# Kernel optimization log

Measured on AMD Instinct MI355X. Metric: run time of the kernel, lower is better.

The kernel has to match this reference:

```python
import jax, jax.numpy as jnp
import numpy as np

NUM_TOKENS = 4096
HIDDEN = 2048
INTER = 1408
NUM_EXPERTS = 8
TOP_K = 2


def setup_inputs() -> dict:
    key = jax.random.key(0)
    k1, k2, k3, k4, k5 = jax.random.split(key, 5)
    hidden_states = jax.random.normal(k1, (NUM_TOKENS, HIDDEN), dtype=jnp.float32)
    # w1: (E, 2*I, H) gate+up fused; w2: (E, H, I)
    w1 = jax.random.normal(k2, (NUM_EXPERTS, 2 * INTER, HIDDEN), dtype=jnp.float32) * (1.0 / np.sqrt(HIDDEN))
    w2 = jax.random.normal(k3, (NUM_EXPERTS, HIDDEN, INTER), dtype=jnp.float32) * (1.0 / np.sqrt(INTER))
    raw = jax.random.uniform(k4, (NUM_TOKENS, TOP_K), dtype=jnp.float32)
    topk_weights = raw / jnp.sum(raw, axis=-1, keepdims=True)  # router softmax-normalized weights
    topk_ids = jax.random.randint(k5, (NUM_TOKENS, TOP_K), 0, NUM_EXPERTS, dtype=jnp.int32)
    return {"hidden_states": hidden_states, "w1": w1, "w2": w2,
            "topk_weights": topk_weights, "topk_ids": topk_ids}


def reference(hidden_states, w1, w2, topk_weights, topk_ids):
    """Math-equivalent of fused_experts (dispatch -> grouped gate_up GEMM ->
    SwiGLU -> grouped down GEMM -> weighted scatter-combine).

    Expressed densely per expert (E is small and fixed), which yields the
    identical output to the sorted/grouped-GEMM formulation.
    """
    E = w1.shape[0]
    inter = w1.shape[1] // 2
    dtype = hidden_states.dtype
    # gate_up projection for every expert: [E, N, 2I]
    gate_up = jnp.einsum('nh,eih->eni', hidden_states, w1)
    gate, up = gate_up[..., :inter], gate_up[..., inter:]
    act = jax.nn.silu(gate) * up  # npu_swiglu: silu(first half) * second half
    # down projection: [E, N, H]
    expert_out = jnp.einsum('eni,ehi->enh', act, w2)
    # combine weight per (token, expert): sum of topk_weights where routed
    one_hot = jax.nn.one_hot(topk_ids, E, dtype=dtype)          # [N, K, E]
    combine = jnp.sum(topk_weights[:, :, None] * one_hot, axis=1)  # [N, E]
    return jnp.einsum('ne,enh->nh', combine, expert_out)
```

## Files before the change

kernel.cpp:

```cpp
#include <hip/hip_runtime.h>
#include <hip/hip_bf16.h>

#define NTOK 4096
#define HID 2048
#define INTER 1408
#define NEXP 8
#define NPAIR 8192
#define NK1 64
#define NK2 44
#define G1SZ 24576
#define G2SZ 16384

typedef short bf16x8 __attribute__((ext_vector_type(8)));
typedef float f32x4 __attribute__((ext_vector_type(4)));

__device__ __forceinline__ unsigned short f2bf(float f) {
  unsigned u = __builtin_bit_cast(unsigned, f);
  u += 0x7fffu + ((u >> 16) & 1u);
  return (unsigned short)(u >> 16);
}
__device__ __forceinline__ float bf2f(unsigned short v) {
  return __builtin_bit_cast(float, (unsigned)v << 16);
}

__device__ __forceinline__ void gload16(const void* g, void* l) {
  __builtin_amdgcn_global_load_lds(
      (const __attribute__((address_space(1))) void*)g,
      (__attribute__((address_space(3))) void*)l, 16, 0, 0);
}

__device__ __forceinline__ int xcd_swz(int lin, int nwg) {
  int xcd = lin & 7, base = lin >> 3;
  int q = nwg >> 3, r = nwg & 7;
  return (xcd < r ? xcd * (q + 1) : r * (q + 1) + (xcd - r) * q) + base;
}

#define BAR __builtin_amdgcn_s_barrier()
#define SCHED0 __builtin_amdgcn_sched_barrier(0)
#define LGKM0 asm volatile("s_waitcnt lgkmcnt(0)" ::: "memory")
#define VM3 asm volatile("s_waitcnt vmcnt(3)" ::: "memory")
#define VM2 asm volatile("s_waitcnt vmcnt(2)" ::: "memory")
#define VM0 asm volatile("s_waitcnt vmcnt(0)" ::: "memory")
#define PRIO1 __builtin_amdgcn_s_setprio(1)
#define PRIO0 __builtin_amdgcn_s_setprio(0)

__global__ void k_prep(const float* __restrict__ hs, const float* __restrict__ w1,
                       unsigned short* __restrict__ dst,
                       const int* __restrict__ ids, int* __restrict__ ctrl,
                       unsigned short* __restrict__ row_token,
                       unsigned short* __restrict__ inv_row) {
  if (blockIdx.x == 0) {
    __shared__ int cnt[NEXP], cur[NEXP];
    int t = threadIdx.x;
    if (t < NEXP) cnt[t] = 0;
    __syncthreads();
    for (int p = t; p < NPAIR; p += 512) atomicAdd(&cnt[ids[p]], 1);
    __syncthreads();
    if (t == 0) {
      int acc = 0, T = 0;
      for (int e = 0; e < NEXP; ++e) {
        cur[e] = acc;
        ctrl[e] = cnt[e];
        ctrl[8 + e] = acc;
        int n = (cnt[e] + 127) >> 7;
        for (int m = 0; m < n; ++m) { ctrl[32 + T] = e; ctrl[104 + T] = m; ++T; }
        acc += cnt[e];
      }
      ctrl[16] = T;
    }
    __syncthreads();
    for (int p = t; p < NPAIR; p += 512) {
      int e = ids[p];
      int pos = atomicAdd(&cur[e], 1);
      row_token[pos] = (unsigned short)(p >> 1);
      inv_row[p] = (unsigned short)pos;
    }
    return;
  }
  const int N0 = NTOK * HID / 4;
  const int N1 = N0 + NEXP * 2 * INTER * HID / 4;
  int stride = (gridDim.x - 1) * 512;
  for (int i = (blockIdx.x - 1) * 512 + threadIdx.x; i < N1; i += stride) {
    const float* s = (i < N0) ? hs : w1;
    int o = (i < N0) ? i : i - N0;
    float4 v = reinterpret_cast<const float4*>(s)[o];
    ushort4 u;
    u.x = f2bf(v.x); u.y = f2bf(v.y); u.z = f2bf(v.z); u.w = f2bf(v.w);
    reinterpret_cast<ushort4*>(dst)[i] = u;
  }
}


#define G1_STAGE(BB, kt) { \
  gload16(aptr + (size_t)(kt)*32, smem + (BB) + wvb16); \
  gload16(bptr0 + (size_t)(kt)*32, smem + (BB) + 8192 + wvb16); \
  gload16(bptr1 + (size_t)(kt)*32, smem + (BB) + 16384 + wvb16); }

#define G1_RD(BB) { \
  _Pragma("unroll") for (int m_ = 0; m_ < 4; ++m_) \
    af[m_] = *(const bf16x8*)(smem + (BB) + arow + m_*1024 + swz); \
  _Pragma("unroll") for (int n_ = 0; n_ < 2; ++n_) { \
    bg[n_] = *(const bf16x8*)(smem + (BB) + brow + n_*1024 + swz); \
    bu[n_] = *(const bf16x8*)(smem + (BB) + brow + 8192 + n_*1024 + swz); } }

#define G1_MMA \
  _Pragma("unroll") for (int m_ = 0; m_ < 4; ++m_) \
  _Pragma("unroll") for (int n_ = 0; n_ < 2; ++n_) { \
    accg[m_][n_] = __builtin_amdgcn_mfma_f32_16x16x32_bf16(af[m_], bg[n_], accg[m_][n_], 0, 0, 0); \
    accu[m_][n_] = __builtin_amdgcn_mfma_f32_16x16x32_bf16(af[m_], bu[n_], accu[m_][n_], 0, 0, 0); }

__global__ __launch_bounds__(512, 4) void k_gemm1(
    const unsigned short* __restrict__ hs,
    const unsigned short* __restrict__ w1,
    const float* __restrict__ w2f,
    unsigned short* __restrict__ w2b,
    const int* __restrict__ ctrl,
    const unsigned short* __restrict__ row_token,
    unsigned short* __restrict__ act) {
  const int T = ctrl[16];
  const int nwg = T * 11;
  const int lin = blockIdx.x;
  if (lin >= nwg) {
    const int NW2 = NEXP * HID * INTER / 4;
    int nc = gridDim.x - nwg;
    for (int i = (lin - nwg) * 512 + threadIdx.x; i < NW2; i += nc * 512) {
      float4 v = reinterpret_cast<const float4*>(w2f)[i];
      ushort4 u;
      u.x = f2bf(v.x); u.y = f2bf(v.y); u.z = f2bf(v.z); u.w = f2bf(v.w);
      reinterpret_cast<ushort4*>(w2b)[i] = u;
    }
    return;
  }
  const int wg = xcd_swz(lin, nwg);
  const int ti = wg / 11;
  const int nt = wg - ti * 11;
  const int e = ctrl[32 + ti], mt = ctrl[104 + ti];
  const int rows = ctrl[e], off_e = ctrl[8 + e];
  const int n0g = nt * 128;
  const unsigned short* w1e = w1 + (size_t)e * (2 * INTER * HID);

  __shared__ __align__(16) char smem[3 * G1SZ];

  const int t = threadIdx.x;
  const int lane = t & 63, wv = t >> 6;
  const int wm = wv >> 2, wn = wv & 3;
  const int lm = lane & 15, hi4 = lane >> 4;
  const int wvb16 = (t & 448) * 16;
  const int arow = wm * 4096 + lm * 64;
  const int brow = 8192 + wn * 2048 + lm * 64;
  const int swz = (hi4 ^ ((lm >> 1) & 3)) * 16;

  const unsigned short *aptr, *bptr0, *bptr1;
  {
    int cl8 = ((t & 3) ^ ((t >> 3) & 3)) * 8;
    int r = t >> 2;
    int g0 = mt * 128 + r; if (g0 > rows - 1) g0 = rows - 1;
    aptr = hs + (size_t)row_token[off_e + g0] * HID + cl8;
    bptr0 = w1e + (size_t)(n0g + r) * HID + cl8;
    bptr1 = w1e + (size_t)(INTER + n0g + r) * HID + cl8;
  }

  f32x4 accg[4][2], accu[4][2];
#pragma unroll
  for (int m = 0; m < 4; ++m)
#pragma unroll
    for (int n = 0; n < 2; ++n) {
      accg[m][n] = (f32x4){0.f, 0.f, 0.f, 0.f};
      accu[m][n] = (f32x4){0.f, 0.f, 0.f, 0.f};
    }
  bf16x8 af[4], bg[2], bu[2];

  unsigned bA = 0, bB = G1SZ, bC = 2 * G1SZ;
  G1_STAGE(bA, 0)
  G1_STAGE(bB, 1)
  VM3; BAR;

  for (int kt = 0; kt < NK1; ++kt) {
    G1_RD(bA)
    if (kt + 2 < NK1) { G1_STAGE(bC, kt + 2) }
    SCHED0;
    PRIO1; G1_MMA PRIO0;
    if (kt < NK1 - 2) { VM3; }
    else if (kt == NK1 - 2) { VM0; }
    LGKM0; BAR;
    unsigned tmp = bA; bA = bB; bB = bC; bC = tmp;
  }

#pragma unroll
  for (int m = 0; m < 4; ++m)
#pragma unroll
    for (int n = 0; n < 2; ++n) {
      int col = n0g + wn * 32 + n * 16 + lm;
#pragma unroll
      for (int j = 0; j < 4; ++j) {
        int grow = mt * 128 + wm * 64 + m * 16 + hi4 * 4 + j;
        if (grow < rows) {
          float g = accg[m][n][j];
          float u = accu[m][n][j];
          float a = g / (1.0f + __expf(-g)) * u;
          act[(size_t)(off_e + grow) * INTER + col] = f2bf(a);
        }
      }
    }
}

#define G2_STAGE(BB, kt) { \
  gload16(aptr + (size_t)(kt)*32, smem + (BB) + wvb16); \
  gload16(bptr + (size_t)(kt)*32, smem + (BB) + 8192 + wvb16); }

#define G2_RD(BB) { \
  _Pragma("unroll") for (int m_ = 0; m_ < 4; ++m_) \
    af[m_] = *(const bf16x8*)(smem + (BB) + arow + m_*1024 + swz); \
  _Pragma("unroll") for (int n_ = 0; n_ < 2; ++n_) \
    bn[n_] = *(const bf16x8*)(smem + (BB) + brow + n_*1024 + swz); }

#define G2_MMA \
  _Pragma("unroll") for (int m_ = 0; m_ < 4; ++m_) \
  _Pragma("unroll") for (int n_ = 0; n_ < 2; ++n_) \
    acc[m_][n_] = __builtin_amdgcn_mfma_f32_16x16x32_bf16(af[m_], bn[n_], acc[m_][n_], 0, 0, 0);

__global__ __launch_bounds__(512, 6) void k_gemm2(
    const unsigned short* __restrict__ act,
    const unsigned short* __restrict__ w2,
    const int* __restrict__ ctrl,
    unsigned short* __restrict__ eo) {
  const int T = ctrl[16];
  const int nwg = T * 16;
  const int lin = blockIdx.x;
  if (lin >= nwg) return;
  const int wg = xcd_swz(lin, nwg);
  const int ti = wg >> 4;
  const int nt = wg & 15;
  const int e = ctrl[32 + ti], mt = ctrl[104 + ti];
  const int rows = ctrl[e], off_e = ctrl[8 + e];
  const int n0 = nt * 128;
  const unsigned short* w2e = w2 + (size_t)e * (HID * INTER);

  __shared__ __align__(16) char smem[3 * G2SZ];

  const int t = threadIdx.x;
  const int lane = t & 63, wv = t >> 6;
  const int wm = wv >> 2, wn = wv & 3;
  const int lm = lane & 15, hi4 = lane >> 4;
  const int wvb16 = (t & 448) * 16;
  const int arow = wm * 4096 + lm * 64;
  const int brow = 8192 + wn * 2048 + lm * 64;
  const int swz = (hi4 ^ ((lm >> 1) & 3)) * 16;

  const unsigned short *aptr, *bptr;
  {
    int cl8 = ((t & 3) ^ ((t >> 3) & 3)) * 8;
    int r = t >> 2;
    int g0 = mt * 128 + r; if (g0 > rows - 1) g0 = rows - 1;
    aptr = act + (size_t)(off_e + g0) * INTER + cl8;
    bptr = w2e + (size_t)(n0 + r) * INTER + cl8;
  }

  f32x4 acc[4][2];
#pragma unroll
  for (int m = 0; m < 4; ++m)
#pragma unroll
    for (int n = 0; n < 2; ++n) acc[m][n] = (f32x4){0.f, 0.f, 0.f, 0.f};
  bf16x8 af[4], bn[2];

  unsigned bA = 0, bB = G2SZ, bC = 2 * G2SZ;
  G2_STAGE(bA, 0)
  G2_STAGE(bB, 1)
  VM2; BAR;

  for (int kt = 0; kt < NK2; ++kt) {
    G2_RD(bA)
    if (kt + 2 < NK2) { G2_STAGE(bC, kt + 2) }
    SCHED0;
    PRIO1; G2_MMA PRIO0;
    if (kt < NK2 - 2) { VM2; }
    else if (kt == NK2 - 2) { VM0; }
    LGKM0; BAR;
    unsigned tmp = bA; bA = bB; bB = bC; bC = tmp;
  }

#pragma unroll
  for (int m = 0; m < 4; ++m)
#pragma unroll
    for (int n = 0; n < 2; ++n) {
      int col = n0 + wn * 32 + n * 16 + lm;
#pragma unroll
      for (int j = 0; j < 4; ++j) {
        int grow = mt * 128 + wm * 64 + m * 16 + hi4 * 4 + j;
        if (grow < rows)
          eo[(size_t)(off_e + grow) * HID + col] = f2bf(acc[m][n][j]);
      }
    }
}

__global__ void k_combine(const unsigned short* __restrict__ eo,
                          const float* __restrict__ tw,
                          const unsigned short* __restrict__ inv_row,
                          float* __restrict__ out) {
  int idx = blockIdx.x * blockDim.x + threadIdx.x;
  int tok = idx >> 8;
  int c8 = (idx & 255) * 8;
  int r0 = inv_row[tok * 2], r1 = inv_row[tok * 2 + 1];
  float w0 = tw[tok * 2], w1 = tw[tok * 2 + 1];
  bf16x8 v0 = *(const bf16x8*)(eo + (size_t)r0 * HID + c8);
  bf16x8 v1 = *(const bf16x8*)(eo + (size_t)r1 * HID + c8);
  float4 o0, o1;
  o0.x = w0 * bf2f((unsigned short)v0[0]) + w1 * bf2f((unsigned short)v1[0]);
  o0.y = w0 * bf2f((unsigned short)v0[1]) + w1 * bf2f((unsigned short)v1[1]);
  o0.z = w0 * bf2f((unsigned short)v0[2]) + w1 * bf2f((unsigned short)v1[2]);
  o0.w = w0 * bf2f((unsigned short)v0[3]) + w1 * bf2f((unsigned short)v1[3]);
  o1.x = w0 * bf2f((unsigned short)v0[4]) + w1 * bf2f((unsigned short)v1[4]);
  o1.y = w0 * bf2f((unsigned short)v0[5]) + w1 * bf2f((unsigned short)v1[5]);
  o1.z = w0 * bf2f((unsigned short)v0[6]) + w1 * bf2f((unsigned short)v1[6]);
  o1.w = w0 * bf2f((unsigned short)v0[7]) + w1 * bf2f((unsigned short)v1[7]);
  float4* op = reinterpret_cast<float4*>(out) + (size_t)tok * 512 + (idx & 255) * 2;
  op[0] = o0;
  op[1] = o1;
}

extern "C" void kernel_launch(void* const* d_in, const int* in_sizes, int n_in,
                              void* d_out, int out_size, void* d_ws, size_t ws_size,
                              hipStream_t stream) {
  const float* hs_f = (const float*)d_in[0];
  const float* w1_f = (const float*)d_in[1];
  const float* w2_f = (const float*)d_in[2];
  const float* tw   = (const float*)d_in[3];
  const int*   tids = (const int*)d_in[4];
  float* out = (float*)d_out;

  char* ws = (char*)d_ws;
  unsigned short* hs_b = (unsigned short*)(ws);
  unsigned short* w2_b = (unsigned short*)(ws + 109051904);
  unsigned short* act  = (unsigned short*)(ws + 155189248);
  unsigned short* eo   = (unsigned short*)(ws + 16777216);
  int* ctrl = (int*)(ws + 178257920);
  unsigned short* row_token = (unsigned short*)(ws + 178258944);
  unsigned short* inv_row   = (unsigned short*)(ws + 178275328);

  k_prep<<<2049, 512, 0, stream>>>(hs_f, w1_f, hs_b, tids, ctrl, row_token, inv_row);

  k_gemm1<<<1280, 512, 0, stream>>>(hs_b, (unsigned short*)(ws + 16777216), w2_f, w2_b,
                                    ctrl, row_token, act);
  k_gemm2<<<72 * 16, 512, 0, stream>>>(act, w2_b, ctrl, eo);
  k_combine<<<NTOK * HID / 8 / 256, 256, 0, stream>>>(eo, tw, inv_row, out);
}
```

Baseline: 263.0 us.

## Double-buffer LDS in grouped GEMMs and widen down-proj tile to 256 columns

Both grouped GEMMs now share one macro-generated main loop. It uses two LDS buffers instead of three and adds a barrier after the fragment reads so the just-read buffer can be refilled. The down-projection kernel computes a 128x256 output tile per workgroup (two B sub-tiles) instead of 128x128, which halves the number of workgroups and reuses each A tile across twice the columns. The cost is an extra barrier per k-step, a shallower prefetch buffer, and lower occupancy and fewer workgroups for GEMM2.

```diff
diff --git a/kernel.cpp b/kernel.cpp
--- a/kernel.cpp
+++ b/kernel.cpp
@@ -9,7 +9,6 @@
 #define NK1 64
 #define NK2 44
 #define G1SZ 24576
-#define G2SZ 16384
 
 typedef short bf16x8 __attribute__((ext_vector_type(8)));
 typedef float f32x4 __attribute__((ext_vector_type(4)));
@@ -39,7 +38,6 @@
 #define SCHED0 __builtin_amdgcn_sched_barrier(0)
 #define LGKM0 asm volatile("s_waitcnt lgkmcnt(0)" ::: "memory")
 #define VM3 asm volatile("s_waitcnt vmcnt(3)" ::: "memory")
-#define VM2 asm volatile("s_waitcnt vmcnt(2)" ::: "memory")
 #define VM0 asm volatile("s_waitcnt vmcnt(0)" ::: "memory")
 #define PRIO1 __builtin_amdgcn_s_setprio(1)
 #define PRIO0 __builtin_amdgcn_s_setprio(0)
@@ -91,23 +89,39 @@
 }
 
 
-#define G1_STAGE(BB, kt) { \
+#define T_STAGE(BB, kt) { \
   gload16(aptr + (size_t)(kt)*32, smem + (BB) + wvb16); \
   gload16(bptr0 + (size_t)(kt)*32, smem + (BB) + 8192 + wvb16); \
   gload16(bptr1 + (size_t)(kt)*32, smem + (BB) + 16384 + wvb16); }
 
-#define G1_RD(BB) { \
+#define T_RD(BB) { \
   _Pragma("unroll") for (int m_ = 0; m_ < 4; ++m_) \
     af[m_] = *(const bf16x8*)(smem + (BB) + arow + m_*1024 + swz); \
   _Pragma("unroll") for (int n_ = 0; n_ < 2; ++n_) { \
-    bg[n_] = *(const bf16x8*)(smem + (BB) + brow + n_*1024 + swz); \
-    bu[n_] = *(const bf16x8*)(smem + (BB) + brow + 8192 + n_*1024 + swz); } }
-
-#define G1_MMA \
+    b0[n_] = *(const bf16x8*)(smem + (BB) + brow + n_*1024 + swz); \
+    b1[n_] = *(const bf16x8*)(smem + (BB) + brow + 8192 + n_*1024 + swz); } }
+
+#define T_MMA \
   _Pragma("unroll") for (int m_ = 0; m_ < 4; ++m_) \
   _Pragma("unroll") for (int n_ = 0; n_ < 2; ++n_) { \
-    accg[m_][n_] = __builtin_amdgcn_mfma_f32_16x16x32_bf16(af[m_], bg[n_], accg[m_][n_], 0, 0, 0); \
-    accu[m_][n_] = __builtin_amdgcn_mfma_f32_16x16x32_bf16(af[m_], bu[n_], accu[m_][n_], 0, 0, 0); }
+    acc0[m_][n_] = __builtin_amdgcn_mfma_f32_16x16x32_bf16(af[m_], b0[n_], acc0[m_][n_], 0, 0, 0); \
+    acc1[m_][n_] = __builtin_amdgcn_mfma_f32_16x16x32_bf16(af[m_], b1[n_], acc1[m_][n_], 0, 0, 0); }
+
+#define T_LOOP(NKT) \
+  T_STAGE(0, 0) \
+  T_STAGE(G1SZ, 1) \
+  VM3; BAR; \
+  unsigned cur = 0, oth = G1SZ; \
+  for (int kt = 0; kt < (NKT); ++kt) { \
+    T_RD(cur) \
+    LGKM0; BAR; \
+    SCHED0; \
+    if (kt + 2 < (NKT)) { T_STAGE(cur, kt + 2) } \
+    PRIO1; T_MMA PRIO0; \
+    if (kt < (NKT) - 2) { VM3; BAR; } \
+    else if (kt == (NKT) - 2) { VM0; BAR; } \
+    unsigned tmp = cur; cur = oth; oth = tmp; \
+  }
 
 __global__ __launch_bounds__(512, 4) void k_gemm1(
     const unsigned short* __restrict__ hs,
@@ -139,7 +153,7 @@
   const int n0g = nt * 128;
   const unsigned short* w1e = w1 + (size_t)e * (2 * INTER * HID);
 
-  __shared__ __align__(16) char smem[3 * G1SZ];
+  __shared__ __align__(16) char smem[2 * G1SZ];
 
   const int t = threadIdx.x;
   const int lane = t & 63, wv = t >> 6;
@@ -160,31 +174,17 @@
     bptr1 = w1e + (size_t)(INTER + n0g + r) * HID + cl8;
   }
 
-  f32x4 accg[4][2], accu[4][2];
+  f32x4 acc0[4][2], acc1[4][2];
 #pragma unroll
   for (int m = 0; m < 4; ++m)
 #pragma unroll
     for (int n = 0; n < 2; ++n) {
-      accg[m][n] = (f32x4){0.f, 0.f, 0.f, 0.f};
-      accu[m][n] = (f32x4){0.f, 0.f, 0.f, 0.f};
-    }
-  bf16x8 af[4], bg[2], bu[2];
-
-  unsigned bA = 0, bB = G1SZ, bC = 2 * G1SZ;
-  G1_STAGE(bA, 0)
-  G1_STAGE(bB, 1)
-  VM3; BAR;
-
-  for (int kt = 0; kt < NK1; ++kt) {
-    G1_RD(bA)
-    if (kt + 2 < NK1) { G1_STAGE(bC, kt + 2) }
-    SCHED0;
-    PRIO1; G1_MMA PRIO0;
-    if (kt < NK1 - 2) { VM3; }
-    else if (kt == NK1 - 2) { VM0; }
-    LGKM0; BAR;
-    unsigned tmp = bA; bA = bB; bB = bC; bC = tmp;
-  }
+      acc0[m][n] = (f32x4){0.f, 0.f, 0.f, 0.f};
+      acc1[m][n] = (f32x4){0.f, 0.f, 0.f, 0.f};
+    }
+  bf16x8 af[4], b0[2], b1[2];
+
+  T_LOOP(NK1)
 
 #pragma unroll
   for (int m = 0; m < 4; ++m)
@@ -195,8 +195,8 @@
       for (int j = 0; j < 4; ++j) {
         int grow = mt * 128 + wm * 64 + m * 16 + hi4 * 4 + j;
         if (grow < rows) {
-          float g = accg[m][n][j];
-          float u = accu[m][n][j];
+          float g = acc0[m][n][j];
+          float u = acc1[m][n][j];
           float a = g / (1.0f + __expf(-g)) * u;
           act[(size_t)(off_e + grow) * INTER + col] = f2bf(a);
         }
@@ -204,39 +204,24 @@
     }
 }
 
-#define G2_STAGE(BB, kt) { \
-  gload16(aptr + (size_t)(kt)*32, smem + (BB) + wvb16); \
-  gload16(bptr + (size_t)(kt)*32, smem + (BB) + 8192 + wvb16); }
-
-#define G2_RD(BB) { \
-  _Pragma("unroll") for (int m_ = 0; m_ < 4; ++m_) \
-    af[m_] = *(const bf16x8*)(smem + (BB) + arow + m_*1024 + swz); \
-  _Pragma("unroll") for (int n_ = 0; n_ < 2; ++n_) \
-    bn[n_] = *(const bf16x8*)(smem + (BB) + brow + n_*1024 + swz); }
-
-#define G2_MMA \
-  _Pragma("unroll") for (int m_ = 0; m_ < 4; ++m_) \
-  _Pragma("unroll") for (int n_ = 0; n_ < 2; ++n_) \
-    acc[m_][n_] = __builtin_amdgcn_mfma_f32_16x16x32_bf16(af[m_], bn[n_], acc[m_][n_], 0, 0, 0);
-
-__global__ __launch_bounds__(512, 6) void k_gemm2(
+__global__ __launch_bounds__(512, 4) void k_gemm2(
     const unsigned short* __restrict__ act,
     const unsigned short* __restrict__ w2,
     const int* __restrict__ ctrl,
     unsigned short* __restrict__ eo) {
   const int T = ctrl[16];
-  const int nwg = T * 16;
+  const int nwg = T * 8;
   const int lin = blockIdx.x;
   if (lin >= nwg) return;
   const int wg = xcd_swz(lin, nwg);
-  const int ti = wg >> 4;
-  const int nt = wg & 15;
+  const int ti = wg >> 3;
+  const int nt = wg & 7;
   const int e = ctrl[32 + ti], mt = ctrl[104 + ti];
   const int rows = ctrl[e], off_e = ctrl[8 + e];
-  const int n0 = nt * 128;
+  const int n0 = nt * 256;
   const unsigned short* w2e = w2 + (size_t)e * (HID * INTER);
 
-  __shared__ __align__(16) char smem[3 * G2SZ];
+  __shared__ __align__(16) char smem[2 * G1SZ];
 
   const int t = threadIdx.x;
   const int lane = t & 63, wv = t >> 6;
@@ -247,37 +232,27 @@
   const int brow = 8192 + wn * 2048 + lm * 64;
   const int swz = (hi4 ^ ((lm >> 1) & 3)) * 16;
 
-  const unsigned short *aptr, *bptr;
+  const unsigned short *aptr, *bptr0, *bptr1;
   {
     int cl8 = ((t & 3) ^ ((t >> 3) & 3)) * 8;
     int r = t >> 2;
     int g0 = mt * 128 + r; if (g0 > rows - 1) g0 = rows - 1;
     aptr = act + (size_t)(off_e + g0) * INTER + cl8;
-    bptr = w2e + (size_t)(n0 + r) * INTER + cl8;
-  }
-
-  f32x4 acc[4][2];
+    bptr0 = w2e + (size_t)(n0 + r) * INTER + cl8;
+    bptr1 = w2e + (size_t)(n0 + 128 + r) * INTER + cl8;
+  }
+
+  f32x4 acc0[4][2], acc1[4][2];
 #pragma unroll
   for (int m = 0; m < 4; ++m)
 #pragma unroll
-    for (int n = 0; n < 2; ++n) acc[m][n] = (f32x4){0.f, 0.f, 0.f, 0.f};
-  bf16x8 af[4], bn[2];
-
-  unsigned bA = 0, bB = G2SZ, bC = 2 * G2SZ;
-  G2_STAGE(bA, 0)
-  G2_STAGE(bB, 1)
-  VM2; BAR;
-
-  for (int kt = 0; kt < NK2; ++kt) {
-    G2_RD(bA)
-    if (kt + 2 < NK2) { G2_STAGE(bC, kt + 2) }
-    SCHED0;
-    PRIO1; G2_MMA PRIO0;
-    if (kt < NK2 - 2) { VM2; }
-    else if (kt == NK2 - 2) { VM0; }
-    LGKM0; BAR;
-    unsigned tmp = bA; bA = bB; bB = bC; bC = tmp;
-  }
+    for (int n = 0; n < 2; ++n) {
+      acc0[m][n] = (f32x4){0.f, 0.f, 0.f, 0.f};
+      acc1[m][n] = (f32x4){0.f, 0.f, 0.f, 0.f};
+    }
+  bf16x8 af[4], b0[2], b1[2];
+
+  T_LOOP(NK2)
 
 #pragma unroll
   for (int m = 0; m < 4; ++m)
@@ -287,8 +262,11 @@
 #pragma unroll
       for (int j = 0; j < 4; ++j) {
         int grow = mt * 128 + wm * 64 + m * 16 + hi4 * 4 + j;
-        if (grow < rows)
-          eo[(size_t)(off_e + grow) * HID + col] = f2bf(acc[m][n][j]);
+        if (grow < rows) {
+          size_t base = (size_t)(off_e + grow) * HID;
+          eo[base + col] = f2bf(acc0[m][n][j]);
+          eo[base + col + 128] = f2bf(acc1[m][n][j]);
+        }
       }
     }
 }
@@ -341,6 +319,6 @@
 
   k_gemm1<<<1280, 512, 0, stream>>>(hs_b, (unsigned short*)(ws + 16777216), w2_f, w2_b,
                                     ctrl, row_token, act);
-  k_gemm2<<<72 * 16, 512, 0, stream>>>(act, w2_b, ctrl, eo);
+  k_gemm2<<<72 * 8, 512, 0, stream>>>(act, w2_b, ctrl, eo);
   k_combine<<<NTOK * HID / 8 / 256, 256, 0, stream>>>(eo, tw, inv_row, out);
 }
```

Measured after the change: 260.7 us. Within noise of the previous version (-0.9%).
